# Kernel tuning notes

Measured on AMD Instinct MI355X. Metric: run time of the kernel, lower is better.

## Reference

```python
import jax, jax.numpy as jnp
import numpy as np

EARLY_ROUND = 6
LATE_ROUND = 12
NUM_CLASSES = 35


def setup_inputs() -> dict:
    key = jax.random.key(0)
    k1, k2, k3 = jax.random.split(key, 3)
    B = 1048576
    logits = jax.random.normal(k1, (B, NUM_CLASSES), dtype=jnp.float32)
    targets = jax.random.randint(k2, (B,), 0, NUM_CLASSES, dtype=jnp.int64)
    turns = jax.random.randint(k3, (B,), 0, 24, dtype=jnp.int64)
    return {"logits": logits, "targets": targets, "turns": turns}


def reference(logits, targets, turns):
    # per-sample cross entropy (reduction='none')
    logp = jax.nn.log_softmax(logits, axis=-1)  # [B, C]
    losses = -jnp.take_along_axis(logp, targets[:, None], axis=-1)[:, 0]  # [B]
    # piecewise-linear weight: 0.7 for turn<=early, 1.0 for turn>=late, lerp between
    t = turns.astype(logits.dtype)
    frac = (t - EARLY_ROUND) / (LATE_ROUND - EARLY_ROUND)
    weights = jnp.clip(0.7 + 0.3 * frac, 0.7, 1.0)
    return jnp.mean(losses * weights)
```

## Files before the change

kernel.cpp:

```cpp
#include <hip/hip_runtime.h>
#include <math.h>

#define NUM_CLASSES 35
#define ROWS_PER_BLOCK 256

__global__ __launch_bounds__(256) void fuzzy_loss_pass1(
    const float* __restrict__ logits,
    const int* __restrict__ targets,
    const int* __restrict__ turns,
    float* __restrict__ block_sums)
{
    __shared__ float lds[ROWS_PER_BLOCK * NUM_CLASSES];
    const int tid  = threadIdx.x;
    const int row0 = blockIdx.x * ROWS_PER_BLOCK;

    {
        const float4* src = (const float4*)(logits + (size_t)row0 * NUM_CLASSES);
        float4* dst = (float4*)lds;
        const int nvec = ROWS_PER_BLOCK * NUM_CLASSES / 4;
        #pragma unroll
        for (int i = 0; i < nvec / ROWS_PER_BLOCK; ++i)
            dst[tid + i * ROWS_PER_BLOCK] = src[tid + i * ROWS_PER_BLOCK];
        {
            int j = 8 * ROWS_PER_BLOCK + tid;
            if (tid < nvec - 8 * ROWS_PER_BLOCK) dst[j] = src[j];
        }
    }
    __syncthreads();

    const int row = row0 + tid;
    const float* r = lds + tid * NUM_CLASSES;

    float s = 0.0f;
    #pragma unroll
    for (int j = 0; j < NUM_CLASSES; ++j) s += __expf(r[j]);

    const int tgt = targets[row];
    const float xt = r[tgt];
    float loss = __logf(s) - xt;

    const float t = (float)turns[row];
    float w = fmaf(0.05f, t, 0.4f);
    w = fminf(fmaxf(w, 0.7f), 1.0f);
    float v = loss * w;

    #pragma unroll
    for (int off = 32; off > 0; off >>= 1)
        v += __shfl_down(v, off, 64);

    __shared__ float wsum[ROWS_PER_BLOCK / 64];
    if ((tid & 63) == 0) wsum[tid >> 6] = v;
    __syncthreads();
    if (tid == 0)
        block_sums[blockIdx.x] = wsum[0] + wsum[1] + wsum[2] + wsum[3];
}

__global__ __launch_bounds__(256) void fuzzy_loss_pass2(
    const float* __restrict__ block_sums,
    float* __restrict__ out,
    int nblocks, float inv_B)
{
    const int tid = threadIdx.x;
    float v = 0.0f;
    const float4* src = (const float4*)block_sums;
    for (int i = tid; i < nblocks / 4; i += 256) {
        float4 f = src[i];
        v += (f.x + f.y) + (f.z + f.w);
    }
    #pragma unroll
    for (int off = 32; off > 0; off >>= 1)
        v += __shfl_down(v, off, 64);

    __shared__ float wsum[4];
    if ((tid & 63) == 0) wsum[tid >> 6] = v;
    __syncthreads();
    if (tid == 0)
        out[0] = (wsum[0] + wsum[1] + wsum[2] + wsum[3]) * inv_B;
}

extern "C" void kernel_launch(void* const* d_in, const int* in_sizes, int n_in,
                              void* d_out, int out_size, void* d_ws, size_t ws_size,
                              hipStream_t stream) {
    const float* logits  = (const float*)d_in[0];
    const int*   targets = (const int*)d_in[1];
    const int*   turns   = (const int*)d_in[2];
    float*       out     = (float*)d_out;
    float*       partial = (float*)d_ws;

    const int B = in_sizes[1];
    const int blocks = B / ROWS_PER_BLOCK;

    fuzzy_loss_pass1<<<blocks, ROWS_PER_BLOCK, 0, stream>>>(logits, targets, turns, partial);
    fuzzy_loss_pass2<<<1, 256, 0, stream>>>(partial, out, blocks, 1.0f / (float)B);
}
```

Baseline: 213.4 us.

## Use persistent wave-private LDS staging with register prefetch of next chunk

Each block now processes four 256-row chunks, and each wave stages its own 64 rows in a private LDS region, so block-wide __syncthreads are no longer needed. The next chunk's logits are prefetched into registers while the current chunk is computed, then written to LDS. The exp sum is split across four accumulators to shorten the dependency chain, and per-wave partials go straight to global memory. The grid is fixed at 1024 blocks, which assumes B equals 1048576 and adds register pressure from the 9-float4 prefetch buffer.

```diff
diff --git a/kernel.cpp b/kernel.cpp
--- a/kernel.cpp
+++ b/kernel.cpp
@@ -2,68 +2,83 @@
 #include <math.h>
 
 #define NUM_CLASSES 35
-#define ROWS_PER_BLOCK 256
+#define CHUNKS 4
+#define NBLOCKS 1024
 
 __global__ __launch_bounds__(256) void fuzzy_loss_pass1(
     const float* __restrict__ logits,
     const int* __restrict__ targets,
     const int* __restrict__ turns,
-    float* __restrict__ block_sums)
+    float* __restrict__ partial)
 {
-    __shared__ float lds[ROWS_PER_BLOCK * NUM_CLASSES];
+    __shared__ float lds[4 * 64 * NUM_CLASSES];
     const int tid  = threadIdx.x;
-    const int row0 = blockIdx.x * ROWS_PER_BLOCK;
+    const int wave = tid >> 6;
+    const int lane = tid & 63;
+    float* wlds = lds + wave * (64 * NUM_CLASSES);
+    const int blk_row0 = blockIdx.x * (256 * CHUNKS);
 
-    {
-        const float4* src = (const float4*)(logits + (size_t)row0 * NUM_CLASSES);
-        float4* dst = (float4*)lds;
-        const int nvec = ROWS_PER_BLOCK * NUM_CLASSES / 4;
+    float4 r[9];
+
+    auto load_chunk = [&](int c) {
+        const float4* g = (const float4*)logits
+                        + ((size_t)(blk_row0 + c * 256 + wave * 64) * NUM_CLASSES) / 4;
         #pragma unroll
-        for (int i = 0; i < nvec / ROWS_PER_BLOCK; ++i)
-            dst[tid + i * ROWS_PER_BLOCK] = src[tid + i * ROWS_PER_BLOCK];
-        {
-            int j = 8 * ROWS_PER_BLOCK + tid;
-            if (tid < nvec - 8 * ROWS_PER_BLOCK) dst[j] = src[j];
+        for (int i = 0; i < 8; ++i) r[i] = g[i * 64 + lane];
+        if (lane < 48) r[8] = g[512 + lane];
+    };
+    auto store_chunk = [&]() {
+        float4* d = (float4*)wlds;
+        #pragma unroll
+        for (int i = 0; i < 8; ++i) d[i * 64 + lane] = r[i];
+        if (lane < 48) d[512 + lane] = r[8];
+    };
+
+    float v = 0.0f;
+    load_chunk(0);
+    store_chunk();
+
+    #pragma unroll
+    for (int c = 0; c < CHUNKS; ++c) {
+        const int row = blk_row0 + c * 256 + wave * 64 + lane;
+        const int   tgt = targets[row];
+        const float t   = (float)turns[row];
+
+        if (c + 1 < CHUNKS) load_chunk(c + 1);
+
+        const float* myrow = wlds + lane * NUM_CLASSES;
+        float s0 = 0.f, s1 = 0.f, s2 = 0.f, s3 = 0.f;
+        #pragma unroll
+        for (int j = 0; j < 32; j += 4) {
+            s0 += __expf(myrow[j]);     s1 += __expf(myrow[j + 1]);
+            s2 += __expf(myrow[j + 2]); s3 += __expf(myrow[j + 3]);
         }
+        s0 += __expf(myrow[32]); s1 += __expf(myrow[33]); s2 += __expf(myrow[34]);
+        const float xt = myrow[tgt];
+        float loss = __logf((s0 + s1) + (s2 + s3)) - xt;
+
+        float w = fmaf(0.05f, t, 0.4f);
+        w = fminf(fmaxf(w, 0.7f), 1.0f);
+        v = fmaf(loss, w, v);
+
+        if (c + 1 < CHUNKS) store_chunk();
     }
-    __syncthreads();
-
-    const int row = row0 + tid;
-    const float* r = lds + tid * NUM_CLASSES;
-
-    float s = 0.0f;
-    #pragma unroll
-    for (int j = 0; j < NUM_CLASSES; ++j) s += __expf(r[j]);
-
-    const int tgt = targets[row];
-    const float xt = r[tgt];
-    float loss = __logf(s) - xt;
-
-    const float t = (float)turns[row];
-    float w = fmaf(0.05f, t, 0.4f);
-    w = fminf(fmaxf(w, 0.7f), 1.0f);
-    float v = loss * w;
 
     #pragma unroll
     for (int off = 32; off > 0; off >>= 1)
         v += __shfl_down(v, off, 64);
-
-    __shared__ float wsum[ROWS_PER_BLOCK / 64];
-    if ((tid & 63) == 0) wsum[tid >> 6] = v;
-    __syncthreads();
-    if (tid == 0)
-        block_sums[blockIdx.x] = wsum[0] + wsum[1] + wsum[2] + wsum[3];
+    if (lane == 0) partial[blockIdx.x * 4 + wave] = v;
 }
 
 __global__ __launch_bounds__(256) void fuzzy_loss_pass2(
-    const float* __restrict__ block_sums,
+    const float* __restrict__ partial,
     float* __restrict__ out,
-    int nblocks, float inv_B)
+    int n, float inv_B)
 {
     const int tid = threadIdx.x;
     float v = 0.0f;
-    const float4* src = (const float4*)block_sums;
-    for (int i = tid; i < nblocks / 4; i += 256) {
+    const float4* src = (const float4*)partial;
+    for (int i = tid; i < n / 4; i += 256) {
         float4 f = src[i];
         v += (f.x + f.y) + (f.z + f.w);
     }
@@ -88,8 +103,7 @@
     float*       partial = (float*)d_ws;
 
     const int B = in_sizes[1];
-    const int blocks = B / ROWS_PER_BLOCK;
 
-    fuzzy_loss_pass1<<<blocks, ROWS_PER_BLOCK, 0, stream>>>(logits, targets, turns, partial);
-    fuzzy_loss_pass2<<<1, 256, 0, stream>>>(partial, out, blocks, 1.0f / (float)B);
+    fuzzy_loss_pass1<<<NBLOCKS, 256, 0, stream>>>(logits, targets, turns, partial);
+    fuzzy_loss_pass2<<<1, 256, 0, stream>>>(partial, out, NBLOCKS * 4, 1.0f / (float)B);
 }
```

Result: slower. 241.0 us (+12.9%).

## Split each row across two threads and write per-wave partials directly

Applied to the files above, without the earlier changes.

Each block now handles 128 rows with 256 threads, two threads per row, each summing 18 exponentials with the shared middle element halved, then combining via xor shuffle. Target and turn loads are issued before the barrier. The block-level LDS reduction and second barrier are removed, and each wave writes its own partial, so pass2 reduces four times as many values. This halves the LDS per block and raises occupancy via launch bounds. The cost is a redundant exp per row, halved loss per thread, and a larger final reduction.

```diff
diff --git a/kernel.cpp b/kernel.cpp
--- a/kernel.cpp
+++ b/kernel.cpp
@@ -2,13 +2,14 @@
 #include <math.h>
 
 #define NUM_CLASSES 35
-#define ROWS_PER_BLOCK 256
+#define ROWS_PER_BLOCK 128
+#define BLOCK 256
 
-__global__ __launch_bounds__(256) void fuzzy_loss_pass1(
+__global__ __launch_bounds__(BLOCK, 8) void fuzzy_loss_pass1(
     const float* __restrict__ logits,
     const int* __restrict__ targets,
     const int* __restrict__ turns,
-    float* __restrict__ block_sums)
+    float* __restrict__ partial)
 {
     __shared__ float lds[ROWS_PER_BLOCK * NUM_CLASSES];
     const int tid  = threadIdx.x;
@@ -17,53 +18,54 @@
     {
         const float4* src = (const float4*)(logits + (size_t)row0 * NUM_CLASSES);
         float4* dst = (float4*)lds;
-        const int nvec = ROWS_PER_BLOCK * NUM_CLASSES / 4;
         #pragma unroll
-        for (int i = 0; i < nvec / ROWS_PER_BLOCK; ++i)
-            dst[tid + i * ROWS_PER_BLOCK] = src[tid + i * ROWS_PER_BLOCK];
-        {
-            int j = 8 * ROWS_PER_BLOCK + tid;
-            if (tid < nvec - 8 * ROWS_PER_BLOCK) dst[j] = src[j];
-        }
+        for (int i = 0; i < 4; ++i)
+            dst[tid + i * BLOCK] = src[tid + i * BLOCK];
+        if (tid < 96) dst[1024 + tid] = src[1024 + tid];
     }
+
+    const int pr   = tid >> 1;
+    const int half = tid & 1;
+    const int row  = row0 + pr;
+    const int tgt  = targets[row];
+    const float t  = (float)turns[row];
+
     __syncthreads();
 
-    const int row = row0 + tid;
-    const float* r = lds + tid * NUM_CLASSES;
+    const float* myrow = lds + pr * NUM_CLASSES;
+    const float* bp = myrow + half * 17;
+    float s0 = 0.f, s1 = 0.f;
+    #pragma unroll
+    for (int k = 0; k < 18; k += 2) {
+        s0 += __expf(bp[k]);
+        s1 += __expf(bp[k + 1]);
+    }
+    float s = (s0 + s1) - 0.5f * __expf(myrow[17]);
+    s += __shfl_xor(s, 1, 64);
 
-    float s = 0.0f;
-    #pragma unroll
-    for (int j = 0; j < NUM_CLASSES; ++j) s += __expf(r[j]);
-
-    const int tgt = targets[row];
-    const float xt = r[tgt];
+    const float xt = myrow[tgt];
     float loss = __logf(s) - xt;
 
-    const float t = (float)turns[row];
     float w = fmaf(0.05f, t, 0.4f);
     w = fminf(fmaxf(w, 0.7f), 1.0f);
-    float v = loss * w;
+    float v = 0.5f * loss * w;
 
     #pragma unroll
     for (int off = 32; off > 0; off >>= 1)
         v += __shfl_down(v, off, 64);
-
-    __shared__ float wsum[ROWS_PER_BLOCK / 64];
-    if ((tid & 63) == 0) wsum[tid >> 6] = v;
-    __syncthreads();
-    if (tid == 0)
-        block_sums[blockIdx.x] = wsum[0] + wsum[1] + wsum[2] + wsum[3];
+    if ((tid & 63) == 0)
+        partial[blockIdx.x * 4 + (tid >> 6)] = v;
 }
 
 __global__ __launch_bounds__(256) void fuzzy_loss_pass2(
-    const float* __restrict__ block_sums,
+    const float* __restrict__ partial,
     float* __restrict__ out,
-    int nblocks, float inv_B)
+    int n, float inv_B)
 {
     const int tid = threadIdx.x;
     float v = 0.0f;
-    const float4* src = (const float4*)block_sums;
-    for (int i = tid; i < nblocks / 4; i += 256) {
+    const float4* src = (const float4*)partial;
+    for (int i = tid; i < n / 4; i += 256) {
         float4 f = src[i];
         v += (f.x + f.y) + (f.z + f.w);
     }
@@ -90,6 +92,6 @@
     const int B = in_sizes[1];
     const int blocks = B / ROWS_PER_BLOCK;
 
-    fuzzy_loss_pass1<<<blocks, ROWS_PER_BLOCK, 0, stream>>>(logits, targets, turns, partial);
-    fuzzy_loss_pass2<<<1, 256, 0, stream>>>(partial, out, blocks, 1.0f / (float)B);
+    fuzzy_loss_pass1<<<blocks, BLOCK, 0, stream>>>(logits, targets, turns, partial);
+    fuzzy_loss_pass2<<<1, 256, 0, stream>>>(partial, out, blocks * 4, 1.0f / (float)B);
 }
```

After: 219.0 us. +2.6%, slower.
